# Kernel optimization log

Measured on AMD Instinct MI355X. Metric: run time of the kernel, lower is better.

The kernel has to match this reference:

```python
import jax, jax.numpy as jnp
import numpy as np

B, J, VN = 256, 140, 14000


def _rodrigues(r):
    # r: [..., 3] axis-angle -> [..., 3, 3] rotation matrices (Rodrigues formula)
    theta = jnp.linalg.norm(r, axis=-1, keepdims=True) + 1e-8  # eps avoids div-by-0 (torch used random eps)
    rh = r / theta
    c = jnp.cos(theta)[..., None]
    s = jnp.sin(theta)[..., None]
    x, y, z = rh[..., 0], rh[..., 1], rh[..., 2]
    zero = jnp.zeros_like(x)
    K = jnp.stack([zero, -z, y, z, zero, -x, -y, x, zero], axis=-1).reshape(r.shape[:-1] + (3, 3))
    eye = jnp.eye(3, dtype=r.dtype)
    outer = rh[..., :, None] * rh[..., None, :]
    return c * eye + (1.0 - c) * outer + s * K


def setup_inputs() -> dict:
    key = jax.random.key(0)
    ks = jax.random.split(key, 8)
    rng = np.random.default_rng(0)
    # kinematic tree: parents[j] < j, parents[0] unused (root)
    parents = np.zeros(J, dtype=np.int64)
    for j in range(1, J):
        parents[j] = rng.integers(0, j)
    init_trans = (rng.normal(size=(J, 3)) * 0.02).astype(np.float32)
    # rest-pose (T-pose) joint locations: FK with identity rotations = prefix sums along tree
    tpose = np.zeros((J, 3), dtype=np.float32)
    tpose[0] = init_trans[0]
    for j in range(1, J):
        tpose[j] = tpose[parents[j]] + init_trans[j]
    pose_rot_vec = jax.random.normal(ks[0], (B, J, 3), dtype=jnp.float32) * 0.1
    pose_trans = jnp.asarray(init_trans)[None] + jax.random.normal(ks[1], (B, J, 3), dtype=jnp.float32) * 0.01
    v_template = jax.random.normal(ks[2], (VN, 3), dtype=jnp.float32)
    w = jax.random.uniform(ks[3], (VN, J), dtype=jnp.float32) ** 8  # peaky, like real skinning weights
    weights = w / jnp.sum(w, axis=1, keepdims=True)
    kp_v_ids = jax.random.randint(ks[4], (22, 4), 0, VN)
    kp_j_ids = jax.random.randint(ks[5], (22, 2), 0, J)
    kp_is_joint = (jnp.arange(22) % 2) == 0
    return {"pose_rot_vec": pose_rot_vec, "pose_trans": pose_trans, "v_template": v_template,
            "weights": weights, "tpose_joints": jnp.asarray(tpose), "parents": jnp.asarray(parents),
            "kp_v_ids": kp_v_ids, "kp_j_ids": kp_j_ids, "kp_is_joint": kp_is_joint}


def reference(pose_rot_vec, pose_trans, v_template, weights, tpose_joints, parents, kp_v_ids, kp_j_ids, kp_is_joint):
    parents_np = np.asarray(parents)  # static tree topology
    b = pose_rot_vec.shape[0]
    R = _rodrigues(pose_rot_vec)  # [B,J,3,3]
    # per-joint local affine S
    S = jnp.zeros((b, J, 4, 4), dtype=pose_rot_vec.dtype)
    S = S.at[:, :, :3, :3].set(R).at[:, :, :3, 3].set(pose_trans).at[:, :, 3, 3].set(1.0)
    # forward kinematics along parent-indexed tree (compute_G)
    Gs = [S[:, 0]]
    for j in range(1, J):
        Gs.append(Gs[int(parents_np[j])] @ S[:, j])
    G = jnp.stack(Gs, axis=1)  # [B,J,4,4]
    J_final = G[:, :, :3, 3]  # get_joints_from_G
    # remove rest-pose joint locations: A = G with t -> t - R_G @ tpose_joint (standard LBS)
    A = G.at[:, :, :3, 3].add(-jnp.einsum('bjmn,jn->bjm', G[:, :, :3, :3], tpose_joints))
    # linear blend skinning
    T = jnp.einsum('vj,bjmn->bvmn', weights, A)  # [B,VN,4,4] blended transforms
    v_h = jnp.concatenate([v_template, jnp.ones((VN, 1), v_template.dtype)], axis=1)  # [VN,4]
    V_final = jnp.einsum('bvmn,vn->bvm', T, v_h)[:, :, :3]  # [B,VN,3]
    # forward_keypoints22: mean-gather over vertex ids ('V') or joint ids ('J')
    kp_v = V_final[:, kp_v_ids].mean(axis=2)  # [B,22,3]
    kp_j = J_final[:, kp_j_ids].mean(axis=2)  # [B,22,3]
    keypoints = jnp.where(kp_is_joint[None, :, None], kp_j, kp_v)
    return V_final, J_final, keypoints
```

## Files before the change

### kernel.cpp

```cpp
#include <hip/hip_runtime.h>

#define B_   256
#define J_   140
#define VN_  14000
#define NKP  22
#define KP   160
#define MP12 3072
#define NSPLIT 32
#define NT   219

#define OFF_J (B_ * VN_ * 3)
#define OFF_K (OFF_J + B_ * J_ * 3)

#define PREPW_BLOCKS ((VN_ * (KP / 8) + 255) / 256)

typedef __attribute__((ext_vector_type(8))) __bf16 bf16x8;
typedef __attribute__((ext_vector_type(4))) float  f32x4;
typedef unsigned int u32;

__device__ __forceinline__ void gload_lds16(const void* g, void* l) {
    __builtin_amdgcn_global_load_lds(
        (const __attribute__((address_space(1))) u32*)g,
        (__attribute__((address_space(3))) u32*)l, 16, 0, 0);
}

__global__ __launch_bounds__(256) void prep_kernel(
    const float* __restrict__ rotvec,
    const float* __restrict__ ptrans,
    const float* __restrict__ tpose,
    const void*  __restrict__ parents_raw,
    const float* __restrict__ w,
    __bf16* __restrict__ Abf,
    __bf16* __restrict__ Wbf,
    float*  __restrict__ Jout)
{
    if (blockIdx.x >= B_) {
        const int id = (blockIdx.x - B_) * 256 + threadIdx.x;
        if (id < VN_ * (KP / 8)) {
            const int v  = id / (KP / 8);
            const int jc = (id % (KP / 8)) * 8;
            __bf16 tmp[8];
            #pragma unroll
            for (int e = 0; e < 8; ++e) {
                const int j = jc + e;
                tmp[e] = (__bf16)((j < J_) ? w[(size_t)v * J_ + j] : 0.0f);
            }
            *reinterpret_cast<int4*>(Wbf + (size_t)v * KP + jc) =
                *reinterpret_cast<int4*>(tmp);
        }
        return;
    }

    __shared__ float sS[J_][12];
    __shared__ float sA[J_][12];
    __shared__ int   sPar[J_];
    __shared__ int   sNz;

    const int b = blockIdx.x;
    const int t = threadIdx.x;

    if (t == 0) sNz = 0;
    __syncthreads();
    const int* p32 = (const int*)parents_raw;
    if (t < J_ / 2 && p32[2 * t + 1] != 0) atomicOr(&sNz, 1);
    __syncthreads();
    const bool is64 = (sNz == 0);

    if (t < J_) {
        const int j = t;
        int p = is64 ? p32[2 * j] : p32[j];
        if (j == 0 || p < 0 || p >= j) p = 0;
        sPar[j] = p;

        const size_t base = ((size_t)b * J_ + j) * 3;
        const float rx = rotvec[base + 0], ry = rotvec[base + 1], rz = rotvec[base + 2];
        const float th  = sqrtf(rx * rx + ry * ry + rz * rz) + 1e-8f;
        const float inv = 1.0f / th;
        const float ux = rx * inv, uy = ry * inv, uz = rz * inv;
        const float c = cosf(th), s = sinf(th);
        const float omc = 1.0f - c;

        sS[j][0]  = c + omc * ux * ux;
        sS[j][1]  = omc * ux * uy - s * uz;
        sS[j][2]  = omc * ux * uz + s * uy;
        sS[j][4]  = omc * uy * ux + s * uz;
        sS[j][5]  = c + omc * uy * uy;
        sS[j][6]  = omc * uy * uz - s * ux;
        sS[j][8]  = omc * uz * ux - s * uy;
        sS[j][9]  = omc * uz * uy + s * ux;
        sS[j][10] = c + omc * uz * uz;
        sS[j][3]  = ptrans[base + 0];
        sS[j][7]  = ptrans[base + 1];
        sS[j][11] = ptrans[base + 2];
    }
    __syncthreads();

    if (t < J_) {
        const int j = t;
        float g[12];
        #pragma unroll
        for (int q = 0; q < 12; ++q) g[q] = sS[j][q];

        int cur = j;
        for (int it = 0; it < J_ && cur != 0; ++it) {
            const int p = sPar[cur];
            float ng[12];
            #pragma unroll
            for (int m = 0; m < 3; ++m) {
                const float s0 = sS[p][m*4+0], s1 = sS[p][m*4+1];
                const float s2 = sS[p][m*4+2], s3 = sS[p][m*4+3];
                #pragma unroll
                for (int cc = 0; cc < 4; ++cc)
                    ng[m*4+cc] = s0 * g[0*4+cc] + s1 * g[1*4+cc] + s2 * g[2*4+cc]
                               + ((cc == 3) ? s3 : 0.0f);
            }
            #pragma unroll
            for (int q = 0; q < 12; ++q) g[q] = ng[q];
            cur = p;
        }

        const float tx = tpose[j*3+0], ty = tpose[j*3+1], tz = tpose[j*3+2];
        #pragma unroll
        for (int m = 0; m < 3; ++m) {
            const float r0 = g[m*4+0], r1 = g[m*4+1], r2 = g[m*4+2];
            const float gt = g[m*4+3];
            sA[j][m*4+0] = r0;
            sA[j][m*4+1] = r1;
            sA[j][m*4+2] = r2;
            sA[j][m*4+3] = gt - (r0 * tx + r1 * ty + r2 * tz);
            Jout[((size_t)b * J_ + j) * 3 + m] = gt;
        }
    }
    __syncthreads();

    for (int idx = t; idx < 12 * KP; idx += 256) {
        const int comp = idx / KP, j = idx % KP;
        const float val = (j < J_) ? sA[j][comp] : 0.0f;
        Abf[((size_t)b * 12 + comp) * KP + j] = (__bf16)val;
    }
}

__global__ __launch_bounds__(256, 2) void gemm_kernel(
    const __bf16* __restrict__ Abf,
    const __bf16* __restrict__ Wbf,
    const float*  __restrict__ vt,
    float* __restrict__ out)
{
    __shared__ __bf16 sB[2][4 * 5 * 64 * 8];
    __shared__ float  sE[4][4][64 * 5];

    const int lane = threadIdx.x & 63;
    const int w    = threadIdx.x >> 6;
    const int r    = lane & 15;
    const int q    = lane >> 4;
    const int q16  = q * 16;
    const int batch0 = blockIdx.y * 16;
    const int rowW   = (batch0 + w * 4) * 12;

    bf16x8 afrag[3][5];
    #pragma unroll
    for (int mi = 0; mi < 3; ++mi) {
        const char* g = (const char*)(Abf + (size_t)(rowW + mi * 16 + r) * KP) + q16;
        #pragma unroll
        for (int s = 0; s < 5; ++s)
            afrag[mi][s] = *reinterpret_cast<const bf16x8*>(g + s * 64);
    }

    {
        int v = blockIdx.x * 64 + w * 16 + r;
        if (v >= VN_) v = VN_ - 1;
        const char* g = (const char*)(Wbf + (size_t)v * KP) + q16;
        char* lb = (char*)&sB[0][0] + w * 5 * 1024;
        #pragma unroll
        for (int s = 0; s < 5; ++s)
            gload_lds16(g + s * 64, lb + s * 1024);
    }
    asm volatile("s_waitcnt vmcnt(0)" ::: "memory");
    __syncthreads();

    int cur = 0;
    for (int t = blockIdx.x; t < NT; t += NSPLIT) {
        const int tn = t + NSPLIT;
        if (tn < NT) {
            int v = tn * 64 + w * 16 + r;
            if (v >= VN_) v = VN_ - 1;
            const char* g = (const char*)(Wbf + (size_t)v * KP) + q16;
            char* lb = (char*)&sB[cur ^ 1][0] + w * 5 * 1024;
            #pragma unroll
            for (int s = 0; s < 5; ++s)
                gload_lds16(g + s * 64, lb + s * 1024);
        }

        f32x4 acc[3][4];
        #pragma unroll
        for (int mi = 0; mi < 3; ++mi)
            #pragma unroll
            for (int f = 0; f < 4; ++f)
                acc[mi][f] = (f32x4){0.f, 0.f, 0.f, 0.f};

        #pragma unroll
        for (int f = 0; f < 4; ++f) {
            #pragma unroll
            for (int s = 0; s < 5; ++s) {
                const bf16x8 bf = *reinterpret_cast<const bf16x8*>(
                    &sB[cur][((f * 5 + s) * 64 + lane) * 8]);
                #pragma unroll
                for (int mi = 0; mi < 3; ++mi)
                    acc[mi][f] = __builtin_amdgcn_mfma_f32_16x16x32_bf16(
                        afrag[mi][s], bf, acc[mi][f], 0, 0, 0);
            }
        }

        const int n0 = t * 64;
        float3 p[4];
        #pragma unroll
        for (int f = 0; f < 4; ++f) {
            const int v  = n0 + f * 16 + r;
            const int vc = (v < VN_) ? v : VN_ - 1;
            p[f] = *reinterpret_cast<const float3*>(vt + 3 * (size_t)vc);
        }
        #pragma unroll
        for (int mi = 0; mi < 3; ++mi) {
            const int mq = mi * 4 + q;
            const int lb = mq / 3;
            const int cg = mq - lb * 3;
            #pragma unroll
            for (int f = 0; f < 4; ++f) {
                const f32x4 c = acc[mi][f];
                sE[w][lb][(f * 16 + r) * 5 + cg] =
                    c[0] * p[f].x + c[1] * p[f].y + c[2] * p[f].z + c[3];
            }
        }
        const int vst = n0 + lane;
        if (vst < VN_) {
            #pragma unroll
            for (int lb = 0; lb < 4; ++lb) {
                const float x = sE[w][lb][lane * 5 + 0];
                const float y = sE[w][lb][lane * 5 + 1];
                const float z = sE[w][lb][lane * 5 + 2];
                float* o = out + ((size_t)(batch0 + w * 4 + lb) * VN_ + vst) * 3;
                o[0] = x; o[1] = y; o[2] = z;
            }
        }

        asm volatile("s_waitcnt vmcnt(0)" ::: "memory");
        __syncthreads();
        cur ^= 1;
    }
}

__global__ __launch_bounds__(256) void kp_kernel(
    const int* __restrict__ kpv, const int* __restrict__ kpj,
    const int* __restrict__ kpb, float* __restrict__ out)
{
    const int i = blockIdx.x * 256 + threadIdx.x;
    if (i >= B_ * NKP) return;
    const int b  = i / NKP;
    const int kk = i - b * NKP;

    float vx, vy, vz;
    if (kpb[kk] != 0) {
        int j0 = kpj[kk * 2 + 0], j1 = kpj[kk * 2 + 1];
        if (j0 < 0 || j0 >= J_) j0 = 0;
        if (j1 < 0 || j1 >= J_) j1 = 0;
        const float* p0 = out + OFF_J + ((size_t)b * J_ + j0) * 3;
        const float* p1 = out + OFF_J + ((size_t)b * J_ + j1) * 3;
        vx = 0.5f * (p0[0] + p1[0]);
        vy = 0.5f * (p0[1] + p1[1]);
        vz = 0.5f * (p0[2] + p1[2]);
    } else {
        vx = vy = vz = 0.0f;
        #pragma unroll
        for (int qq = 0; qq < 4; ++qq) {
            int vid = kpv[kk * 4 + qq];
            if (vid < 0 || vid >= VN_) vid = 0;
            const float* p = out + ((size_t)b * VN_ + vid) * 3;
            vx += p[0]; vy += p[1]; vz += p[2];
        }
        vx *= 0.25f; vy *= 0.25f; vz *= 0.25f;
    }
    float* o = out + OFF_K + ((size_t)b * NKP + kk) * 3;
    o[0] = vx; o[1] = vy; o[2] = vz;
}

extern "C" void kernel_launch(void* const* d_in, const int* in_sizes, int n_in,
                              void* d_out, int out_size, void* d_ws, size_t ws_size,
                              hipStream_t stream) {
    const float* rotvec  = (const float*)d_in[0];
    const float* ptrans  = (const float*)d_in[1];
    const float* vt      = (const float*)d_in[2];
    const float* w       = (const float*)d_in[3];
    const float* tpose   = (const float*)d_in[4];
    const void*  parents = (const void*)d_in[5];
    const int*   kpv     = (const int*)d_in[6];
    const int*   kpj     = (const int*)d_in[7];
    const int*   kpb     = (const int*)d_in[8];

    float*  out = (float*)d_out;
    __bf16* Abf = (__bf16*)d_ws;
    __bf16* Wbf = (__bf16*)((char*)d_ws + (size_t)MP12 * KP * 2);

    prep_kernel<<<B_ + PREPW_BLOCKS, 256, 0, stream>>>(
        rotvec, ptrans, tpose, parents, w, Abf, Wbf, out + OFF_J);

    dim3 grid(NSPLIT, MP12 / 192);
    gemm_kernel<<<grid, 256, 0, stream>>>(Abf, Wbf, vt, out);

    kp_kernel<<<(B_ * NKP + 255) / 256, 256, 0, stream>>>(kpv, kpj, kpb, out);
}
```

Measured before the change: 36.50 us.

## Fuse keypoint computation into prep and GEMM kernels, drop separate launch

Removes the standalone keypoint kernel. Joint-based keypoints are now computed in prep_kernel from shared-memory joint positions, and vertex-based keypoints are zero-initialised there. The GEMM blocks that own each referenced vertex tile then add their contributions with atomicAdd after the main loop. This saves one kernel launch and its global re-reads, at the cost of float atomics with a non-deterministic summation order. It also relies on each block reading back its own earlier global writes of the vertex outputs.

```diff
diff --git a/kernel.cpp b/kernel.cpp
--- a/kernel.cpp
+++ b/kernel.cpp
@@ -30,9 +30,11 @@
     const float* __restrict__ tpose,
     const void*  __restrict__ parents_raw,
     const float* __restrict__ w,
+    const int*   __restrict__ kpj,
+    const int*   __restrict__ kpb,
     __bf16* __restrict__ Abf,
     __bf16* __restrict__ Wbf,
-    float*  __restrict__ Jout)
+    float*  __restrict__ out)
 {
     if (blockIdx.x >= B_) {
         const int id = (blockIdx.x - B_) * 256 + threadIdx.x;
@@ -53,6 +55,7 @@
 
     __shared__ float sS[J_][12];
     __shared__ float sA[J_][12];
+    __shared__ float sJ3[J_][3];
     __shared__ int   sPar[J_];
     __shared__ int   sNz;
 
@@ -128,7 +131,8 @@
             sA[j][m*4+1] = r1;
             sA[j][m*4+2] = r2;
             sA[j][m*4+3] = gt - (r0 * tx + r1 * ty + r2 * tz);
-            Jout[((size_t)b * J_ + j) * 3 + m] = gt;
+            sJ3[j][m]    = gt;
+            out[OFF_J + ((size_t)b * J_ + j) * 3 + m] = gt;
         }
     }
     __syncthreads();
@@ -138,12 +142,29 @@
         const float val = (j < J_) ? sA[j][comp] : 0.0f;
         Abf[((size_t)b * 12 + comp) * KP + j] = (__bf16)val;
     }
+
+    if (t < NKP) {
+        const int kk = t;
+        float* o = out + OFF_K + ((size_t)b * NKP + kk) * 3;
+        if (kpb[kk] != 0) {
+            int j0 = kpj[kk * 2 + 0], j1 = kpj[kk * 2 + 1];
+            if (j0 < 0 || j0 >= J_) j0 = 0;
+            if (j1 < 0 || j1 >= J_) j1 = 0;
+            o[0] = 0.5f * (sJ3[j0][0] + sJ3[j1][0]);
+            o[1] = 0.5f * (sJ3[j0][1] + sJ3[j1][1]);
+            o[2] = 0.5f * (sJ3[j0][2] + sJ3[j1][2]);
+        } else {
+            o[0] = 0.0f; o[1] = 0.0f; o[2] = 0.0f;
+        }
+    }
 }
 
 __global__ __launch_bounds__(256, 2) void gemm_kernel(
     const __bf16* __restrict__ Abf,
     const __bf16* __restrict__ Wbf,
     const float*  __restrict__ vt,
+    const int*    __restrict__ kpv,
+    const int*    __restrict__ kpb,
     float* __restrict__ out)
 {
     __shared__ __bf16 sB[2][4 * 5 * 64 * 8];
@@ -154,6 +175,7 @@
     const int r    = lane & 15;
     const int q    = lane >> 4;
     const int q16  = q * 16;
+    const int bx     = blockIdx.x;
     const int batch0 = blockIdx.y * 16;
     const int rowW   = (batch0 + w * 4) * 12;
 
@@ -167,7 +189,7 @@
     }
 
     {
-        int v = blockIdx.x * 64 + w * 16 + r;
+        int v = bx * 64 + w * 16 + r;
         if (v >= VN_) v = VN_ - 1;
         const char* g = (const char*)(Wbf + (size_t)v * KP) + q16;
         char* lb = (char*)&sB[0][0] + w * 5 * 1024;
@@ -179,7 +201,7 @@
     __syncthreads();
 
     int cur = 0;
-    for (int t = blockIdx.x; t < NT; t += NSPLIT) {
+    for (int t = bx; t < NT; t += NSPLIT) {
         const int tn = t + NSPLIT;
         if (tn < NT) {
             int v = tn * 64 + w * 16 + r;
@@ -247,40 +269,25 @@
         __syncthreads();
         cur ^= 1;
     }
-}
-
-__global__ __launch_bounds__(256) void kp_kernel(
-    const int* __restrict__ kpv, const int* __restrict__ kpj,
-    const int* __restrict__ kpb, float* __restrict__ out)
-{
-    const int i = blockIdx.x * 256 + threadIdx.x;
-    if (i >= B_ * NKP) return;
-    const int b  = i / NKP;
-    const int kk = i - b * NKP;
-
-    float vx, vy, vz;
-    if (kpb[kk] != 0) {
-        int j0 = kpj[kk * 2 + 0], j1 = kpj[kk * 2 + 1];
-        if (j0 < 0 || j0 >= J_) j0 = 0;
-        if (j1 < 0 || j1 >= J_) j1 = 0;
-        const float* p0 = out + OFF_J + ((size_t)b * J_ + j0) * 3;
-        const float* p1 = out + OFF_J + ((size_t)b * J_ + j1) * 3;
-        vx = 0.5f * (p0[0] + p1[0]);
-        vy = 0.5f * (p0[1] + p1[1]);
-        vz = 0.5f * (p0[2] + p1[2]);
-    } else {
-        vx = vy = vz = 0.0f;
-        #pragma unroll
-        for (int qq = 0; qq < 4; ++qq) {
+
+    {
+        const int nTasks = NKP * 4 * 16;
+        for (int task = threadIdx.x; task < nTasks; task += 256) {
+            const int lb16 = task & 15;
+            const int e    = task >> 4;
+            const int kk = e >> 2, qq = e & 3;
+            if (kpb[kk] != 0) continue;
             int vid = kpv[kk * 4 + qq];
             if (vid < 0 || vid >= VN_) vid = 0;
-            const float* p = out + ((size_t)b * VN_ + vid) * 3;
-            vx += p[0]; vy += p[1]; vz += p[2];
-        }
-        vx *= 0.25f; vy *= 0.25f; vz *= 0.25f;
-    }
-    float* o = out + OFF_K + ((size_t)b * NKP + kk) * 3;
-    o[0] = vx; o[1] = vy; o[2] = vz;
+            if (((vid >> 6) & 31) != bx) continue;
+            const int bb = batch0 + lb16;
+            const float* pv = out + ((size_t)bb * VN_ + vid) * 3;
+            float* o = out + OFF_K + ((size_t)bb * NKP + kk) * 3;
+            atomicAdd(&o[0], 0.25f * pv[0]);
+            atomicAdd(&o[1], 0.25f * pv[1]);
+            atomicAdd(&o[2], 0.25f * pv[2]);
+        }
+    }
 }
 
 extern "C" void kernel_launch(void* const* d_in, const int* in_sizes, int n_in,
@@ -301,10 +308,8 @@
     __bf16* Wbf = (__bf16*)((char*)d_ws + (size_t)MP12 * KP * 2);
 
     prep_kernel<<<B_ + PREPW_BLOCKS, 256, 0, stream>>>(
-        rotvec, ptrans, tpose, parents, w, Abf, Wbf, out + OFF_J);
+        rotvec, ptrans, tpose, parents, w, kpj, kpb, Abf, Wbf, out);
 
     dim3 grid(NSPLIT, MP12 / 192);
-    gemm_kernel<<<grid, 256, 0, stream>>>(Abf, Wbf, vt, out);
-
-    kp_kernel<<<(B_ * NKP + 255) / 256, 256, 0, stream>>>(kpv, kpj, kpb, out);
+    gemm_kernel<<<grid, 256, 0, stream>>>(Abf, Wbf, vt, kpv, kpb, out);
 }
```

New measurement: 37.53 us. +2.8%, slower.

## Keep vertex weight fragments in registers and loop batch groups per block

Applied to the files above, without the earlier changes.

Restructures the skinning GEMM so each block owns one 64-vertex tile, loads its bf16 weight fragments and template vertices once into registers, and iterates over four 16-batch groups, reading joint transform fragments directly from global. This removes the LDS double-buffer, async global-to-LDS loads and per-tile barriers, and launches many more blocks. In exchange, each wave loads the same weight fragments redundantly and reloads A fragments per batch group from cache.

```diff
diff --git a/kernel.cpp b/kernel.cpp
--- a/kernel.cpp
+++ b/kernel.cpp
@@ -6,7 +6,6 @@
 #define NKP  22
 #define KP   160
 #define MP12 3072
-#define NSPLIT 32
 #define NT   219
 
 #define OFF_J (B_ * VN_ * 3)
@@ -17,12 +16,6 @@
 typedef __attribute__((ext_vector_type(8))) __bf16 bf16x8;
 typedef __attribute__((ext_vector_type(4))) float  f32x4;
 typedef unsigned int u32;
-
-__device__ __forceinline__ void gload_lds16(const void* g, void* l) {
-    __builtin_amdgcn_global_load_lds(
-        (const __attribute__((address_space(1))) u32*)g,
-        (__attribute__((address_space(3))) u32*)l, 16, 0, 0);
-}
 
 __global__ __launch_bounds__(256) void prep_kernel(
     const float* __restrict__ rotvec,
@@ -146,49 +139,47 @@
     const float*  __restrict__ vt,
     float* __restrict__ out)
 {
-    __shared__ __bf16 sB[2][4 * 5 * 64 * 8];
-    __shared__ float  sE[4][4][64 * 5];
+    __shared__ float sE[4][4][64 * 5];
 
     const int lane = threadIdx.x & 63;
     const int w    = threadIdx.x >> 6;
     const int r    = lane & 15;
     const int q    = lane >> 4;
     const int q16  = q * 16;
-    const int batch0 = blockIdx.y * 16;
-    const int rowW   = (batch0 + w * 4) * 12;
-
-    bf16x8 afrag[3][5];
+    const int n0     = blockIdx.x * 64;
+    const int batchY = blockIdx.y * 64;
+
+    bf16x8 bfrag[4][5];
     #pragma unroll
-    for (int mi = 0; mi < 3; ++mi) {
-        const char* g = (const char*)(Abf + (size_t)(rowW + mi * 16 + r) * KP) + q16;
-        #pragma unroll
-        for (int s = 0; s < 5; ++s)
-            afrag[mi][s] = *reinterpret_cast<const bf16x8*>(g + s * 64);
-    }
-
-    {
-        int v = blockIdx.x * 64 + w * 16 + r;
+    for (int f = 0; f < 4; ++f) {
+        int v = n0 + f * 16 + r;
         if (v >= VN_) v = VN_ - 1;
         const char* g = (const char*)(Wbf + (size_t)v * KP) + q16;
-        char* lb = (char*)&sB[0][0] + w * 5 * 1024;
         #pragma unroll
         for (int s = 0; s < 5; ++s)
-            gload_lds16(g + s * 64, lb + s * 1024);
-    }
-    asm volatile("s_waitcnt vmcnt(0)" ::: "memory");
-    __syncthreads();
-
-    int cur = 0;
-    for (int t = blockIdx.x; t < NT; t += NSPLIT) {
-        const int tn = t + NSPLIT;
-        if (tn < NT) {
-            int v = tn * 64 + w * 16 + r;
-            if (v >= VN_) v = VN_ - 1;
-            const char* g = (const char*)(Wbf + (size_t)v * KP) + q16;
-            char* lb = (char*)&sB[cur ^ 1][0] + w * 5 * 1024;
+            bfrag[f][s] = *reinterpret_cast<const bf16x8*>(g + s * 64);
+    }
+
+    float3 p[4];
+    #pragma unroll
+    for (int f = 0; f < 4; ++f) {
+        const int v  = n0 + f * 16 + r;
+        const int vc = (v < VN_) ? v : VN_ - 1;
+        p[f] = *reinterpret_cast<const float3*>(vt + 3 * (size_t)vc);
+    }
+    const int vst = n0 + lane;
+
+    for (int bg = 0; bg < 4; ++bg) {
+        const int batch0 = batchY + bg * 16;
+        const int rowW   = (batch0 + w * 4) * 12;
+
+        bf16x8 afrag[3][5];
+        #pragma unroll
+        for (int mi = 0; mi < 3; ++mi) {
+            const char* g = (const char*)(Abf + (size_t)(rowW + mi * 16 + r) * KP) + q16;
             #pragma unroll
             for (int s = 0; s < 5; ++s)
-                gload_lds16(g + s * 64, lb + s * 1024);
+                afrag[mi][s] = *reinterpret_cast<const bf16x8*>(g + s * 64);
         }
 
         f32x4 acc[3][4];
@@ -202,23 +193,13 @@
         for (int f = 0; f < 4; ++f) {
             #pragma unroll
             for (int s = 0; s < 5; ++s) {
-                const bf16x8 bf = *reinterpret_cast<const bf16x8*>(
-                    &sB[cur][((f * 5 + s) * 64 + lane) * 8]);
                 #pragma unroll
                 for (int mi = 0; mi < 3; ++mi)
                     acc[mi][f] = __builtin_amdgcn_mfma_f32_16x16x32_bf16(
-                        afrag[mi][s], bf, acc[mi][f], 0, 0, 0);
-            }
-        }
-
-        const int n0 = t * 64;
-        float3 p[4];
-        #pragma unroll
-        for (int f = 0; f < 4; ++f) {
-            const int v  = n0 + f * 16 + r;
-            const int vc = (v < VN_) ? v : VN_ - 1;
-            p[f] = *reinterpret_cast<const float3*>(vt + 3 * (size_t)vc);
-        }
+                        afrag[mi][s], bfrag[f][s], acc[mi][f], 0, 0, 0);
+            }
+        }
+
         #pragma unroll
         for (int mi = 0; mi < 3; ++mi) {
             const int mq = mi * 4 + q;
@@ -231,7 +212,6 @@
                     c[0] * p[f].x + c[1] * p[f].y + c[2] * p[f].z + c[3];
             }
         }
-        const int vst = n0 + lane;
         if (vst < VN_) {
             #pragma unroll
             for (int lb = 0; lb < 4; ++lb) {
@@ -242,10 +222,6 @@
                 o[0] = x; o[1] = y; o[2] = z;
             }
         }
-
-        asm volatile("s_waitcnt vmcnt(0)" ::: "memory");
-        __syncthreads();
-        cur ^= 1;
     }
 }
 
@@ -303,7 +279,7 @@
     prep_kernel<<<B_ + PREPW_BLOCKS, 256, 0, stream>>>(
         rotvec, ptrans, tpose, parents, w, Abf, Wbf, out + OFF_J);
 
-    dim3 grid(NSPLIT, MP12 / 192);
+    dim3 grid(NT, 4);
     gemm_kernel<<<grid, 256, 0, stream>>>(Abf, Wbf, vt, out);
 
     kp_kernel<<<(B_ * NKP + 255) / 256, 256, 0, stream>>>(kpv, kpj, kpb, out);
```

Result: slower. 50.27 us (+37.7%).
